# Kernel optimization log

Measured on AMD Instinct MI355X. Metric: run time of the kernel, lower is better.

Reference implementation:

```python
import jax, jax.numpy as jnp
import numpy as np

NUM_SHARDS = 512
NUM_CLUSTERS = 256
INPUT_SIZE = 1024
OUTPUT_SIZE = 1024
BATCH = 1024
INIT_RANGE = 0.1


def setup_inputs() -> dict:
    key0 = jax.random.key(0)
    k1, k2, k3, k4, k5 = jax.random.split(key0, 5)
    shard = jax.random.randint(k1, (BATCH,), 0, NUM_SHARDS)
    key = jax.random.normal(k2, (BATCH, INPUT_SIZE), dtype=jnp.float32)
    # Embedding tables, uniform(-init_range, init_range) as in the torch module
    latent_vars = jax.random.uniform(k3, (NUM_SHARDS, NUM_CLUSTERS * OUTPUT_SIZE),
                                     minval=-INIT_RANGE, maxval=INIT_RANGE, dtype=jnp.float32)
    weight = jax.random.uniform(k4, (NUM_SHARDS, INPUT_SIZE * NUM_CLUSTERS),
                                minval=-INIT_RANGE, maxval=INIT_RANGE, dtype=jnp.float32)
    bias = jax.random.uniform(k5, (NUM_SHARDS, NUM_CLUSTERS),
                              minval=-INIT_RANGE, maxval=INIT_RANGE, dtype=jnp.float32)
    return {"shard": shard, "key": key, "latent_vars": latent_vars,
            "weight": weight, "bias": bias}


def reference(shard, key, latent_vars, weight, bias):
    B = key.shape[0]
    # Gather per-sample parameters
    lat = latent_vars[shard].reshape(B, NUM_CLUSTERS, OUTPUT_SIZE)   # [B, C, O]
    w = weight[shard].reshape(B, INPUT_SIZE, NUM_CLUSTERS)           # [B, I, C]
    b = bias[shard]                                                  # [B, C]
    # logit = key^T @ W + b  (batched vec-mat)
    logit = jnp.einsum('bi,bic->bc', key, w) + b                     # [B, C]
    prob = jax.nn.softmax(logit, axis=1)                             # [B, C]
    # lat_h = prob @ lat  (batched vec-mat combine)
    lat_h = jnp.einsum('bc,bco->bo', prob, lat)                      # [B, O]
    return (lat_h, prob)
```

## Files before the change

kernel.cpp:

```cpp
#include <hip/hip_runtime.h>

#define NSH 512
#define NC  256
#define NI  1024
#define NO  1024
#define NB  1024
#define NMAX 8
#define UF  8

__global__ __launch_bounds__(512) void group_kernel(const int* __restrict__ shard,
                                                    int* __restrict__ order,
                                                    int* __restrict__ base,
                                                    int* __restrict__ cnt) {
    __shared__ int h[NSH];
    __shared__ int woff[8];
    __shared__ int cur[NSH];
    const int tid  = threadIdx.x;
    const int lane = tid & 63;
    const int w8   = tid >> 6;
    h[tid] = 0;
    __syncthreads();
    for (int i = tid; i < NB; i += 512) atomicAdd(&h[shard[i]], 1);
    __syncthreads();
    const int v = h[tid];
    int inc = v;
    #pragma unroll
    for (int off = 1; off < 64; off <<= 1) {
        int t = __shfl_up(inc, off, 64);
        if (lane >= off) inc += t;
    }
    if (lane == 63) woff[w8] = inc;
    __syncthreads();
    if (tid == 0) {
        int a = 0;
        #pragma unroll
        for (int i = 0; i < 8; ++i) { int t = woff[i]; woff[i] = a; a += t; }
    }
    __syncthreads();
    const int b0 = woff[w8] + inc - v;
    base[tid] = b0;
    cnt[tid]  = v;
    cur[tid]  = b0;
    __syncthreads();
    for (int i = tid; i < NB; i += 512) {
        int pos = atomicAdd(&cur[shard[i]], 1);
        order[pos] = i;
    }
}

__global__ __launch_bounds__(512, 2) void mega_kernel(
        const int*   __restrict__ order,
        const int*   __restrict__ base,
        const int*   __restrict__ cnt,
        const float* __restrict__ key,
        const float* __restrict__ wgt,
        const float* __restrict__ lat,
        const float* __restrict__ bias,
        float*       __restrict__ outq,
        float*       __restrict__ outp) {
    const int s     = blockIdx.x;
    const int n_tot = cnt[s];
    if (n_tot == 0) return;
    const int b0   = base[s];
    const int tid  = threadIdx.x;
    const int w    = tid >> 6;
    const int lane = tid & 63;
    const int c4   = lane << 2;

    const float* __restrict__ Wp = wgt + (size_t)s * (NI * NC);
    const float* __restrict__ Lp = lat + (size_t)s * (NC * NO);

    __shared__ float key_s[NMAX][NI];
    __shared__ float red[4096];
    __shared__ float prob_s[NMAX][NC];
    __shared__ float bias_s[NC];
    __shared__ float xm[2][4];
    __shared__ float xs[2][4];
    __shared__ int   samp_s[NMAX];

    if (tid < 64)
        *(float4*)&bias_s[tid << 2] =
            *(const float4*)(bias + (size_t)s * NC + (tid << 2));

    for (int p0 = 0; p0 < n_tot; p0 += NMAX) {
        const int n = min(NMAX, n_tot - p0);
        __syncthreads();
        if (tid < n) samp_s[tid] = order[b0 + p0 + tid];
        __syncthreads();

        for (int idx = tid; idx < NMAX * (NI / 4); idx += 512) {
            const int ns = idx >> 8;
            const int e4 = idx & 255;
            float4 v = make_float4(0.f, 0.f, 0.f, 0.f);
            if (ns < n)
                v = *(const float4*)(key + (size_t)samp_s[ns] * NI + (e4 << 2));
            *(float4*)&key_s[ns][e4 << 2] = v;
        }
        __syncthreads();

        float4 acc[NMAX];
        #pragma unroll
        for (int j = 0; j < NMAX; ++j) acc[j] = make_float4(0.f, 0.f, 0.f, 0.f);

        #pragma unroll 1
        for (int k0 = 0; k0 < 128; k0 += UF) {
            float4 wv[UF];
            #pragma unroll
            for (int u = 0; u < UF; ++u)
                wv[u] = *(const float4*)(Wp + (size_t)(w + 8 * (k0 + u)) * NC + c4);
            #pragma unroll
            for (int u = 0; u < UF; ++u) {
                const int il = w + 8 * (k0 + u);
                #pragma unroll
                for (int j = 0; j < NMAX; ++j) {
                    const float k = key_s[j][il];
                    acc[j].x = fmaf(k, wv[u].x, acc[j].x);
                    acc[j].y = fmaf(k, wv[u].y, acc[j].y);
                    acc[j].z = fmaf(k, wv[u].z, acc[j].z);
                    acc[j].w = fmaf(k, wv[u].w, acc[j].w);
                }
            }
        }

        const int half = tid >> 8;
        const int w3   = w & 3;
        const int cc   = tid & 255;
        #pragma unroll
        for (int r = 0; r < 4; ++r) {
            __syncthreads();
            *(float4*)&red[w * 512 + c4]       = acc[2 * r];
            *(float4*)&red[w * 512 + 256 + c4] = acc[2 * r + 1];
            __syncthreads();
            const int j = 2 * r + half;
            float lg = -1e30f;
            if (j < n) {
                lg = bias_s[cc];
                #pragma unroll
                for (int ww = 0; ww < 8; ++ww)
                    lg += red[ww * 512 + half * 256 + cc];
            }
            float m = lg;
            #pragma unroll
            for (int off = 32; off >= 1; off >>= 1)
                m = fmaxf(m, __shfl_xor(m, off, 64));
            if (lane == 0) xm[half][w3] = m;
            __syncthreads();
            m = fmaxf(fmaxf(xm[half][0], xm[half][1]),
                      fmaxf(xm[half][2], xm[half][3]));
            const float e = __expf(lg - m);
            float sm = e;
            #pragma unroll
            for (int off = 32; off >= 1; off >>= 1)
                sm += __shfl_xor(sm, off, 64);
            if (lane == 0) xs[half][w3] = sm;
            __syncthreads();
            sm = xs[half][0] + xs[half][1] + xs[half][2] + xs[half][3];
            const float p = e / sm;
            if (j < n) {
                prob_s[j][cc] = p;
                outq[(size_t)samp_s[j] * NC + cc] = p;
            } else {
                prob_s[j][cc] = 0.f;
            }
        }
        __syncthreads();

        const int oc = w & 3;
        const int cp = w >> 2;
        const int ob = oc << 8;
        float4 acc2[NMAX];
        #pragma unroll
        for (int j = 0; j < NMAX; ++j) acc2[j] = make_float4(0.f, 0.f, 0.f, 0.f);

        #pragma unroll 1
        for (int k0 = 0; k0 < 128; k0 += UF) {
            float4 lv[UF];
            #pragma unroll
            for (int u = 0; u < UF; ++u) {
                const int c = cp + 2 * (k0 + u);
                lv[u] = *(const float4*)(Lp + (size_t)c * NO + ob + c4);
            }
            #pragma unroll
            for (int u = 0; u < UF; ++u) {
                const int c = cp + 2 * (k0 + u);
                #pragma unroll
                for (int j = 0; j < NMAX; ++j) {
                    const float p = prob_s[j][c];
                    acc2[j].x = fmaf(p, lv[u].x, acc2[j].x);
                    acc2[j].y = fmaf(p, lv[u].y, acc2[j].y);
                    acc2[j].z = fmaf(p, lv[u].z, acc2[j].z);
                    acc2[j].w = fmaf(p, lv[u].w, acc2[j].w);
                }
            }
        }

        #pragma unroll
        for (int r = 0; r < 4; ++r) {
            __syncthreads();
            *(float4*)&red[cp * 2048 + ob + c4]        = acc2[2 * r];
            *(float4*)&red[cp * 2048 + 1024 + ob + c4] = acc2[2 * r + 1];
            __syncthreads();
            #pragma unroll
            for (int q = 0; q < 4; ++q) {
                const int flat = (q << 9) | tid;
                const int sel  = flat >> 10;
                const int o    = flat & 1023;
                const int j    = 2 * r + sel;
                if (j < n)
                    outp[(size_t)samp_s[j] * NO + o] =
                        red[sel * 1024 + o] + red[2048 + sel * 1024 + o];
            }
        }
    }
}

extern "C" void kernel_launch(void* const* d_in, const int* in_sizes, int n_in,
                              void* d_out, int out_size, void* d_ws, size_t ws_size,
                              hipStream_t stream) {
    const int*   shard = (const int*)  d_in[0];
    const float* key   = (const float*)d_in[1];
    const float* lat   = (const float*)d_in[2];
    const float* wgt   = (const float*)d_in[3];
    const float* bias  = (const float*)d_in[4];

    float* outp = (float*)d_out;
    float* outq = (float*)d_out + (size_t)NB * NO;

    int* order = (int*)d_ws;
    int* base  = order + NB;
    int* cnt   = base + NSH;

    group_kernel<<<1,   512, 0, stream>>>(shard, order, base, cnt);
    mega_kernel <<<NSH, 512, 0, stream>>>(order, base, cnt, key, wgt, lat, bias,
                                          outq, outp);
}
```

Baseline: 197.7 us.

## Fold shard grouping into main kernel and use contiguous per-wave row ranges

Drops the separate single-block grouping kernel. Each block now scans the shard array itself and collects its own sample indices in shared memory with an atomic counter, which removes one launch and the serial dependency on a one-block kernel. It also changes the per-wave row assignment in both vec-mat loops from strided rows to a contiguous block of 128 rows per wave, which should improve locality and prefetching. The costs are a redundant 1024-element scan in each of the 512 blocks and 4KB of extra shared memory per block, and the within-shard sample order now follows atomic order rather than being deterministic.

```diff
diff --git a/kernel.cpp b/kernel.cpp
--- a/kernel.cpp
+++ b/kernel.cpp
@@ -8,75 +8,44 @@
 #define NMAX 8
 #define UF  8
 
-__global__ __launch_bounds__(512) void group_kernel(const int* __restrict__ shard,
-                                                    int* __restrict__ order,
-                                                    int* __restrict__ base,
-                                                    int* __restrict__ cnt) {
-    __shared__ int h[NSH];
-    __shared__ int woff[8];
-    __shared__ int cur[NSH];
-    const int tid  = threadIdx.x;
-    const int lane = tid & 63;
-    const int w8   = tid >> 6;
-    h[tid] = 0;
-    __syncthreads();
-    for (int i = tid; i < NB; i += 512) atomicAdd(&h[shard[i]], 1);
-    __syncthreads();
-    const int v = h[tid];
-    int inc = v;
-    #pragma unroll
-    for (int off = 1; off < 64; off <<= 1) {
-        int t = __shfl_up(inc, off, 64);
-        if (lane >= off) inc += t;
-    }
-    if (lane == 63) woff[w8] = inc;
-    __syncthreads();
-    if (tid == 0) {
-        int a = 0;
-        #pragma unroll
-        for (int i = 0; i < 8; ++i) { int t = woff[i]; woff[i] = a; a += t; }
-    }
-    __syncthreads();
-    const int b0 = woff[w8] + inc - v;
-    base[tid] = b0;
-    cnt[tid]  = v;
-    cur[tid]  = b0;
-    __syncthreads();
-    for (int i = tid; i < NB; i += 512) {
-        int pos = atomicAdd(&cur[shard[i]], 1);
-        order[pos] = i;
-    }
-}
-
 __global__ __launch_bounds__(512, 2) void mega_kernel(
-        const int*   __restrict__ order,
-        const int*   __restrict__ base,
-        const int*   __restrict__ cnt,
+        const int*   __restrict__ shard,
         const float* __restrict__ key,
         const float* __restrict__ wgt,
         const float* __restrict__ lat,
         const float* __restrict__ bias,
         float*       __restrict__ outq,
         float*       __restrict__ outp) {
-    const int s     = blockIdx.x;
-    const int n_tot = cnt[s];
-    if (n_tot == 0) return;
-    const int b0   = base[s];
+    const int s    = blockIdx.x;
     const int tid  = threadIdx.x;
     const int w    = tid >> 6;
     const int lane = tid & 63;
     const int c4   = lane << 2;
 
-    const float* __restrict__ Wp = wgt + (size_t)s * (NI * NC);
-    const float* __restrict__ Lp = lat + (size_t)s * (NC * NO);
-
     __shared__ float key_s[NMAX][NI];
     __shared__ float red[4096];
     __shared__ float prob_s[NMAX][NC];
     __shared__ float bias_s[NC];
+    __shared__ int   samp_all[NB];
     __shared__ float xm[2][4];
     __shared__ float xs[2][4];
     __shared__ int   samp_s[NMAX];
+    __shared__ int   cnt_s;
+
+    if (tid == 0) cnt_s = 0;
+    __syncthreads();
+    for (int i = tid; i < NB; i += 512) {
+        if (shard[i] == s) {
+            int p = atomicAdd(&cnt_s, 1);
+            samp_all[p] = i;
+        }
+    }
+    __syncthreads();
+    const int n_tot = cnt_s;
+    if (n_tot == 0) return;
+
+    const float* __restrict__ Wp = wgt + (size_t)s * (NI * NC);
+    const float* __restrict__ Lp = lat + (size_t)s * (NC * NO);
 
     if (tid < 64)
         *(float4*)&bias_s[tid << 2] =
@@ -85,7 +54,7 @@
     for (int p0 = 0; p0 < n_tot; p0 += NMAX) {
         const int n = min(NMAX, n_tot - p0);
         __syncthreads();
-        if (tid < n) samp_s[tid] = order[b0 + p0 + tid];
+        if (tid < n) samp_s[tid] = samp_all[p0 + tid];
         __syncthreads();
 
         for (int idx = tid; idx < NMAX * (NI / 4); idx += 512) {
@@ -102,15 +71,16 @@
         #pragma unroll
         for (int j = 0; j < NMAX; ++j) acc[j] = make_float4(0.f, 0.f, 0.f, 0.f);
 
+        const int rowA = w << 7;
         #pragma unroll 1
         for (int k0 = 0; k0 < 128; k0 += UF) {
             float4 wv[UF];
             #pragma unroll
             for (int u = 0; u < UF; ++u)
-                wv[u] = *(const float4*)(Wp + (size_t)(w + 8 * (k0 + u)) * NC + c4);
+                wv[u] = *(const float4*)(Wp + (size_t)(rowA + k0 + u) * NC + c4);
             #pragma unroll
             for (int u = 0; u < UF; ++u) {
-                const int il = w + 8 * (k0 + u);
+                const int il = rowA + k0 + u;
                 #pragma unroll
                 for (int j = 0; j < NMAX; ++j) {
                     const float k = key_s[j][il];
@@ -168,6 +138,7 @@
         const int oc = w & 3;
         const int cp = w >> 2;
         const int ob = oc << 8;
+        const int rowB = cp << 7;
         float4 acc2[NMAX];
         #pragma unroll
         for (int j = 0; j < NMAX; ++j) acc2[j] = make_float4(0.f, 0.f, 0.f, 0.f);
@@ -177,12 +148,12 @@
             float4 lv[UF];
             #pragma unroll
             for (int u = 0; u < UF; ++u) {
-                const int c = cp + 2 * (k0 + u);
+                const int c = rowB + k0 + u;
                 lv[u] = *(const float4*)(Lp + (size_t)c * NO + ob + c4);
             }
             #pragma unroll
             for (int u = 0; u < UF; ++u) {
-                const int c = cp + 2 * (k0 + u);
+                const int c = rowB + k0 + u;
                 #pragma unroll
                 for (int j = 0; j < NMAX; ++j) {
                     const float p = prob_s[j][c];
@@ -226,11 +197,5 @@
     float* outp = (float*)d_out;
     float* outq = (float*)d_out + (size_t)NB * NO;
 
-    int* order = (int*)d_ws;
-    int* base  = order + NB;
-    int* cnt   = base + NSH;
-
-    group_kernel<<<1,   512, 0, stream>>>(shard, order, base, cnt);
-    mega_kernel <<<NSH, 512, 0, stream>>>(order, base, cnt, key, wgt, lat, bias,
-                                          outq, outp);
+    mega_kernel<<<NSH, 512, 0, stream>>>(shard, key, wgt, lat, bias, outq, outp);
 }
```

Result: no change. 195.3 us (-1.2%).
